# Optimization experiments

Hardware: AMD Instinct MI355X
Metric: run time of the kernel (lower is better)

Reference implementation:

```python
import jax, jax.numpy as jnp
import numpy as np

IN_DIM, H1, H2, N_CLASSES = 128, 100, 128, 19
BATCH, SEQ = 512, 256


def _lstm_relu(x, W, U, b, units):
    """Keras LSTM with activation='relu', recurrent_activation='sigmoid'.
    x: [B, T, D]. Returns (all hidden states [B, T, units], last hidden [B, units]).
    Gate order (Keras): i, f, g(cell candidate), o.
    """
    B = x.shape[0]
    h0 = jnp.zeros((B, units), x.dtype)
    c0 = jnp.zeros((B, units), x.dtype)

    # precompute input projections for all timesteps: [T, B, 4*units]
    zx = jnp.einsum('btd,dk->tbk', x, W) + b

    def step(carry, zx_t):
        h, c = carry
        z = zx_t + h @ U
        i, f, g, o = jnp.split(z, 4, axis=-1)
        i = jax.nn.sigmoid(i)
        f = jax.nn.sigmoid(f)
        g = jax.nn.relu(g)          # activation='relu'
        o = jax.nn.sigmoid(o)
        c = f * c + i * g
        h = o * jax.nn.relu(c)      # output activation is also relu
        return (h, c), h

    (h_last, _), hs = jax.lax.scan(step, (h0, c0), zx)
    return jnp.transpose(hs, (1, 0, 2)), h_last


def setup_inputs() -> dict:
    key = jax.random.key(0)
    ks = jax.random.split(key, 9)
    def w(k, shape, fan_in):
        return jax.random.normal(k, shape, jnp.float32) / np.sqrt(fan_in)
    x = jax.random.normal(ks[0], (BATCH, SEQ, IN_DIM), jnp.float32)
    return {
        'x': x,
        'W1': w(ks[1], (IN_DIM, 4 * H1), IN_DIM),
        'U1': w(ks[2], (H1, 4 * H1), H1),
        'b1': jnp.zeros((4 * H1,), jnp.float32),
        'W2': w(ks[3], (H1, 4 * H2), H1),
        'U2': w(ks[4], (H2, 4 * H2), H2),
        'b2': jnp.zeros((4 * H2,), jnp.float32),
        'Wd': w(ks[5], (H2, N_CLASSES), H2),
        'bd': jnp.zeros((N_CLASSES,), jnp.float32),
    }


def reference(x, W1, U1, b1, W2, U2, b2, Wd, bd):
    h1_seq, _ = _lstm_relu(x, W1, U1, b1, H1)      # [B, T, 100]
    _, h2 = _lstm_relu(h1_seq, W2, U2, b2, H2)     # [B, 128] (last step only)
    logits = h2 @ Wd + bd
    return jax.nn.softmax(logits, axis=-1)         # [B, 19]
```

## Files before the change

### kernel.cpp

```cpp
#include <hip/hip_runtime.h>
#include <math.h>


#define T_SEQ 256
#define BATCH 512
#define IN_DIM 128
#define H1 100
#define H2 128
#define NCLS 19

typedef float f4v __attribute__((ext_vector_type(4)));

__device__ __forceinline__ float sigmoidf_(float x) {
    return 1.0f / (1.0f + __expf(-x));
}
__device__ __forceinline__ float hsum4_(f4v v) {
    return (v.x + v.y) + (v.z + v.w);
}

#define REP8(M)  M(0) M(1) M(2) M(3) M(4) M(5) M(6) M(7)
#define REP25(M) M(0) M(1) M(2) M(3) M(4) M(5) M(6) M(7) M(8) M(9) M(10) M(11) \
                 M(12) M(13) M(14) M(15) M(16) M(17) M(18) M(19) M(20) M(21) M(22) M(23) M(24)

template<int K, int N, bool SWAP>
__global__ __launch_bounds__(256, 2)
void proj_kernel(const float* __restrict__ A, const float* __restrict__ W,
                 const float* __restrict__ bias, float* __restrict__ out)
{
    constexpr int LD = 132;
    __shared__ __align__(16) float As[32 * LD];
    __shared__ __align__(16) float Ws[32 * LD];
    const int tid = threadIdx.x;
    const int r0 = blockIdx.x * 128;
    const int c0 = blockIdx.y * 128;
    const int ty = tid >> 4, tx = tid & 15;

#define PACC(i) f4v accL##i = {0.f,0.f,0.f,0.f}; f4v accR##i = {0.f,0.f,0.f,0.f};
    REP8(PACC)
#undef PACC

    for (int kk = 0; kk < K; kk += 32) {
        __syncthreads();
#pragma unroll
        for (int i = 0; i < 4; ++i) {
            int idx = tid + i * 256;
            int row = idx >> 3, kg = idx & 7;
            int k = kk + kg * 4;
            f4v v = {0.f, 0.f, 0.f, 0.f};
            if (k < K) v = *(const f4v*)&A[(size_t)(r0 + row) * K + k];
            As[(kg * 4 + 0) * LD + row] = v.x;
            As[(kg * 4 + 1) * LD + row] = v.y;
            As[(kg * 4 + 2) * LD + row] = v.z;
            As[(kg * 4 + 3) * LD + row] = v.w;
        }
#pragma unroll
        for (int i = 0; i < 4; ++i) {
            int idx = tid + i * 256;
            int k = idx >> 5, cg = idx & 31;
            int gk = kk + k, gc = c0 + cg * 4;
            f4v v = {0.f, 0.f, 0.f, 0.f};
            if (gk < K && gc < N) v = *(const f4v*)&W[(size_t)gk * N + gc];
            *(f4v*)&Ws[k * LD + cg * 4] = v;
        }
        __syncthreads();
#pragma unroll
        for (int k = 0; k < 32; ++k) {
            f4v av0 = *(const f4v*)&As[k * LD + ty * 8];
            f4v av1 = *(const f4v*)&As[k * LD + ty * 8 + 4];
            f4v b0v = *(const f4v*)&Ws[k * LD + tx * 8];
            f4v b1v = *(const f4v*)&Ws[k * LD + tx * 8 + 4];
#define PFMA(i, s) accL##i += (s) * b0v; accR##i += (s) * b1v;
            PFMA(0, av0.x) PFMA(1, av0.y) PFMA(2, av0.z) PFMA(3, av0.w)
            PFMA(4, av1.x) PFMA(5, av1.y) PFMA(6, av1.z) PFMA(7, av1.w)
#undef PFMA
        }
    }

    const int cb = c0 + tx * 8;
    float b0 = (cb + 0 < N) ? bias[cb + 0] : 0.f;
    float b1 = (cb + 1 < N) ? bias[cb + 1] : 0.f;
    float b2 = (cb + 2 < N) ? bias[cb + 2] : 0.f;
    float b3 = (cb + 3 < N) ? bias[cb + 3] : 0.f;
    float b4 = (cb + 4 < N) ? bias[cb + 4] : 0.f;
    float b5 = (cb + 5 < N) ? bias[cb + 5] : 0.f;
    float b6 = (cb + 6 < N) ? bias[cb + 6] : 0.f;
    float b7 = (cb + 7 < N) ? bias[cb + 7] : 0.f;
    f4v bL = {b0, b1, b2, b3};
    f4v bR = {b4, b5, b6, b7};
#define PST(i) { \
        int r = r0 + ty * 8 + i; \
        size_t orow = SWAP ? ((size_t)(r & 255) * BATCH + (r >> 8)) : (size_t)r; \
        if (cb < N)     { f4v v = accL##i + bL; *(f4v*)&out[orow * N + cb] = v; } \
        if (cb + 4 < N) { f4v v = accR##i + bR; *(f4v*)&out[orow * N + cb + 4] = v; } }
    REP8(PST)
#undef PST
}

__global__ __launch_bounds__(256)
__attribute__((amdgpu_waves_per_eu(1, 1)))
void rec1_kernel(const float* __restrict__ zx,
                 const float* __restrict__ U1,
                 float* __restrict__ h1seq)
{
    const int row = blockIdx.x;
    const int k = threadIdx.x;
    __shared__ __align__(16) float hs[H1];
    __shared__ __align__(8) float fo[2 * H1];

    const int kk = (k < 200) ? k : 0;
    const int c0 = kk, c1 = kk + 200;

#define R1_LD(i) \
    f4v u0_##i, u1_##i; { \
        const float* p = U1 + (4 * i) * 400; \
        u0_##i = (f4v){p[c0], p[400 + c0], p[800 + c0], p[1200 + c0]}; \
        u1_##i = (f4v){p[c1], p[400 + c1], p[800 + c1], p[1200 + c1]}; }
    REP25(R1_LD)
#undef R1_LD

    if (k < H1) hs[k] = 0.0f;
    float cst = 0.0f;
    float zc0 = zx[(size_t)row * 400 + c0];
    float zc1 = zx[(size_t)row * 400 + c1];
    __syncthreads();

    for (int t = 0; t < T_SEQ; ++t) {
        int tn = (t + 1 < T_SEQ) ? t + 1 : t;
        const float* pz = &zx[((size_t)tn * BATCH + row) * 400];
        float zn0 = pz[c0];
        float zn1 = pz[c1];

        f4v s0 = {0.f, 0.f, 0.f, 0.f};
        f4v s1 = {0.f, 0.f, 0.f, 0.f};
#define R1_FMA(i) { f4v hv = *(const f4v*)&hs[4 * i]; s0 += hv * u0_##i; s1 += hv * u1_##i; }
        REP25(R1_FMA)
#undef R1_FMA
        float a0 = sigmoidf_(zc0 + hsum4_(s0));
        float a1h = zc1 + hsum4_(s1);
        float a1 = (k < H1) ? fmaxf(a1h, 0.0f) : sigmoidf_(a1h);
        if (k >= H1 && k < 200) *(float2*)&fo[2 * (k - H1)] = make_float2(a0, a1);
        __syncthreads();

        if (k < H1) {
            float2 f_o = *(const float2*)&fo[2 * k];
            cst = f_o.x * cst + a0 * a1;
            float h = f_o.y * fmaxf(cst, 0.0f);
            hs[k] = h;
            h1seq[((size_t)t * BATCH + row) * H1 + k] = h;
        }
        __syncthreads();
        zc0 = zn0;
        zc1 = zn1;
    }
}

template<bool INIT, bool LAST>
__global__ __launch_bounds__(512)
__attribute__((amdgpu_waves_per_eu(2, 2)))
void rec2_chunk(const float* __restrict__ zx,
                const float* __restrict__ U2,
                float* __restrict__ cbuf,
                float* __restrict__ hbuf,
                float* __restrict__ h2out,
                int tlen)
{
    const int row = blockIdx.x;
    const int tid = threadIdx.x;
    const int kq = tid >> 7;
    const int cl = tid & 127;
    __shared__ __align__(16) float hs[H2];
    __shared__ float zp[4 * 512];
    __shared__ float za[512];

#define R2_LD(j) \
    f4v w0_##j, w1_##j, w2_##j, w3_##j; { \
        const float* p = U2 + (size_t)(kq * 32 + 4 * j) * 512 + cl; \
        w0_##j = (f4v){p[0],   p[512],       p[1024],       p[1536]}; \
        w1_##j = (f4v){p[128], p[512 + 128], p[1024 + 128], p[1536 + 128]}; \
        w2_##j = (f4v){p[256], p[512 + 256], p[1024 + 256], p[1536 + 256]}; \
        w3_##j = (f4v){p[384], p[512 + 384], p[1024 + 384], p[1536 + 384]}; }
    REP8(R2_LD)
#undef R2_LD

    float cst = 0.0f;
    if (tid < H2) {
        if (INIT) {
            hs[tid] = 0.0f;
        } else {
            hs[tid] = hbuf[(size_t)row * H2 + tid];
            cst = cbuf[(size_t)row * H2 + tid];
        }
    }
    float zc = zx[(size_t)row * 512 + tid];
    __syncthreads();

    for (int t = 0; t < tlen; ++t) {
        int tn = (t + 1 < tlen) ? t + 1 : t;
        float zn = zx[((size_t)tn * BATCH + row) * 512 + tid];

        f4v s0 = {0.f, 0.f, 0.f, 0.f};
        f4v s1 = {0.f, 0.f, 0.f, 0.f};
        f4v s2 = {0.f, 0.f, 0.f, 0.f};
        f4v s3 = {0.f, 0.f, 0.f, 0.f};
#define R2_FMA(j) { f4v hv = *(const f4v*)&hs[kq * 32 + 4 * j]; \
        s0 += hv * w0_##j; s1 += hv * w1_##j; s2 += hv * w2_##j; s3 += hv * w3_##j; }
        REP8(R2_FMA)
#undef R2_FMA
        zp[kq * 512 + cl]       = hsum4_(s0);
        zp[kq * 512 + cl + 128] = hsum4_(s1);
        zp[kq * 512 + cl + 256] = hsum4_(s2);
        zp[kq * 512 + cl + 384] = hsum4_(s3);
        __syncthreads();

        float z = zc + (zp[tid] + zp[512 + tid]) + (zp[1024 + tid] + zp[1536 + tid]);
        float a = (tid >= 2 * H2 && tid < 3 * H2) ? fmaxf(z, 0.0f) : sigmoidf_(z);
        za[tid] = a;
        __syncthreads();

        if (tid < H2) {
            float i = za[tid], f = za[tid + 128], g = za[tid + 256], o = za[tid + 384];
            cst = f * cst + i * g;
            hs[tid] = o * fmaxf(cst, 0.0f);
        }
        __syncthreads();
        zc = zn;
    }

    if (tid < H2) {
        float h = hs[tid];
        cbuf[(size_t)row * H2 + tid] = cst;
        hbuf[(size_t)row * H2 + tid] = h;
        if (LAST) h2out[(size_t)row * H2 + tid] = h;
    }
}

__global__ __launch_bounds__(64, 1)
void dense_softmax_kernel(const float* __restrict__ h2, const float* __restrict__ Wd,
                          const float* __restrict__ bd, float* __restrict__ out)
{
    const int b = blockIdx.x;
    const int k = threadIdx.x;
    __shared__ __align__(16) float hsm[H2];
    if (k < H2 / 4) ((f4v*)hsm)[k] = ((const f4v*)(h2 + (size_t)b * H2))[k];
    __syncthreads();

    float logit = -1e30f;
    if (k < NCLS) {
        float acc = bd[k];
#pragma unroll
        for (int d = 0; d < H2; ++d) acc += hsm[d] * Wd[d * NCLS + k];
        logit = acc;
    }
    float m = logit;
#pragma unroll
    for (int off = 32; off >= 1; off >>= 1) m = fmaxf(m, __shfl_xor(m, off, 64));
    float e = (k < NCLS) ? __expf(logit - m) : 0.0f;
    float s = e;
#pragma unroll
    for (int off = 32; off >= 1; off >>= 1) s += __shfl_xor(s, off, 64);
    if (k < NCLS) out[(size_t)b * NCLS + k] = e / s;
}

__global__ __launch_bounds__(448, 1)
void lstm1_fb(const float* __restrict__ x, const float* __restrict__ W1,
              const float* __restrict__ U1, const float* __restrict__ b1,
              float* __restrict__ h1out)
{
    const int b = blockIdx.x;
    const int k = threadIdx.x;
    __shared__ __align__(16) float xs[IN_DIM];
    __shared__ __align__(16) float hs[H1];
    __shared__ __align__(16) float zs[4 * H1];
    float w1r[IN_DIM];
    float u1r[H1];
    float bias = 0.0f;
    if (k < 4 * H1) {
        bias = b1[k];
#pragma unroll
        for (int d = 0; d < IN_DIM; ++d) w1r[d] = W1[d * (4 * H1) + k];
#pragma unroll
        for (int j = 0; j < H1; ++j) u1r[j] = U1[j * (4 * H1) + k];
    }
    if (k < H1) hs[k] = 0.0f;
    if (k < IN_DIM / 4)
        ((float4*)xs)[k] = ((const float4*)(x + ((size_t)b * T_SEQ) * IN_DIM))[k];
    float c = 0.0f;
    __syncthreads();
    for (int t = 0; t < T_SEQ; ++t) {
        if (k < 4 * H1) {
            float acc0 = bias, acc1 = 0.f, acc2 = 0.f, acc3 = 0.f;
#pragma unroll
            for (int q = 0; q < IN_DIM / 4; ++q) {
                float4 xv = ((const float4*)xs)[q];
                acc0 += xv.x * w1r[4 * q]; acc1 += xv.y * w1r[4 * q + 1];
                acc2 += xv.z * w1r[4 * q + 2]; acc3 += xv.w * w1r[4 * q + 3];
            }
#pragma unroll
            for (int q = 0; q < H1 / 4; ++q) {
                float4 hv = ((const float4*)hs)[q];
                acc0 += hv.x * u1r[4 * q]; acc1 += hv.y * u1r[4 * q + 1];
                acc2 += hv.z * u1r[4 * q + 2]; acc3 += hv.w * u1r[4 * q + 3];
            }
            float zv = (acc0 + acc1) + (acc2 + acc3);
            zs[k] = (k >= 2 * H1 && k < 3 * H1) ? fmaxf(zv, 0.0f) : sigmoidf_(zv);
        }
        __syncthreads();
        if (k < H1) {
            float i = zs[k], f = zs[k + H1], g = zs[k + 2 * H1], o = zs[k + 3 * H1];
            c = f * c + i * g;
            float h = o * fmaxf(c, 0.0f);
            hs[k] = h;
            h1out[((size_t)t * BATCH + b) * H1 + k] = h;
        }
        int tn = t + 1;
        if (tn < T_SEQ && k < IN_DIM / 4)
            ((float4*)xs)[k] = ((const float4*)(x + ((size_t)b * T_SEQ + tn) * IN_DIM))[k];
        __syncthreads();
    }
}

__global__ __launch_bounds__(512, 1)
void lstm2_fb(const float* __restrict__ h1in, const float* __restrict__ W2,
              const float* __restrict__ U2, const float* __restrict__ b2,
              float* __restrict__ h2out)
{
    const int b = blockIdx.x;
    const int k = threadIdx.x;
    __shared__ __align__(16) float ps[H1];
    __shared__ __align__(16) float hs[H2];
    __shared__ __align__(16) float zs[4 * H2];
    float w2r[H1];
    float u2r[H2];
    float bias = b2[k];
#pragma unroll
    for (int j = 0; j < H1; ++j) w2r[j] = W2[j * (4 * H2) + k];
#pragma unroll
    for (int j = 0; j < H2; ++j) u2r[j] = U2[j * (4 * H2) + k];
    if (k < H2) hs[k] = 0.0f;
    if (k < H1 / 4)
        ((float4*)ps)[k] = ((const float4*)(h1in + (size_t)b * H1))[k];
    float c = 0.0f;
    float hlast = 0.0f;
    __syncthreads();
    for (int t = 0; t < T_SEQ; ++t) {
        float acc0 = bias, acc1 = 0.f, acc2 = 0.f, acc3 = 0.f;
#pragma unroll
        for (int q = 0; q < H1 / 4; ++q) {
            float4 pv = ((const float4*)ps)[q];
            acc0 += pv.x * w2r[4 * q]; acc1 += pv.y * w2r[4 * q + 1];
            acc2 += pv.z * w2r[4 * q + 2]; acc3 += pv.w * w2r[4 * q + 3];
        }
#pragma unroll
        for (int q = 0; q < H2 / 4; ++q) {
            float4 hv = ((const float4*)hs)[q];
            acc0 += hv.x * u2r[4 * q]; acc1 += hv.y * u2r[4 * q + 1];
            acc2 += hv.z * u2r[4 * q + 2]; acc3 += hv.w * u2r[4 * q + 3];
        }
        float zv = (acc0 + acc1) + (acc2 + acc3);
        zs[k] = (k >= 2 * H2 && k < 3 * H2) ? fmaxf(zv, 0.0f) : sigmoidf_(zv);
        __syncthreads();
        if (k < H2) {
            float i = zs[k], f = zs[k + H2], g = zs[k + 2 * H2], o = zs[k + 3 * H2];
            c = f * c + i * g;
            hlast = o * fmaxf(c, 0.0f);
            hs[k] = hlast;
        }
        int tn = t + 1;
        if (tn < T_SEQ && k < H1 / 4)
            ((float4*)ps)[k] = ((const float4*)(h1in + ((size_t)tn * BATCH + b) * H1))[k];
        __syncthreads();
    }
    if (k < H2) h2out[(size_t)b * H2 + k] = hlast;
}

extern "C" void kernel_launch(void* const* d_in, const int* in_sizes, int n_in,
                              void* d_out, int out_size, void* d_ws, size_t ws_size,
                              hipStream_t stream) {
    const float* x  = (const float*)d_in[0];
    const float* W1 = (const float*)d_in[1];
    const float* U1 = (const float*)d_in[2];
    const float* b1 = (const float*)d_in[3];
    const float* W2 = (const float*)d_in[4];
    const float* U2 = (const float*)d_in[5];
    const float* b2 = (const float*)d_in[6];
    const float* Wd = (const float*)d_in[7];
    const float* bd = (const float*)d_in[8];
    float* out = (float*)d_out;

    const size_t zx_elems = (size_t)T_SEQ * BATCH * 400;
    const size_t h1_elems = (size_t)T_SEQ * BATCH * H1;
    const size_t st_elems = (size_t)BATCH * H2;
    const size_t need = (zx_elems + h1_elems + 3 * st_elems) * sizeof(float);

    if (ws_size >= need) {
        float* zxbuf = (float*)d_ws;
        float* h1buf = zxbuf + zx_elems;
        float* cbuf  = h1buf + h1_elems;
        float* hbuf  = cbuf + st_elems;
        float* h2buf = hbuf + st_elems;
        const int TC = T_SEQ / 2;

        hipLaunchKernelGGL((proj_kernel<IN_DIM, 4 * H1, true>), dim3(1024, 4), dim3(256), 0, stream,
                           x, W1, b1, zxbuf);
        hipLaunchKernelGGL(rec1_kernel, dim3(BATCH), dim3(256), 0, stream,
                           zxbuf, U1, h1buf);
        hipLaunchKernelGGL((proj_kernel<H1, 4 * H2, false>), dim3(512, 4), dim3(256), 0, stream,
                           h1buf, W2, b2, zxbuf);
        hipLaunchKernelGGL((rec2_chunk<true, false>), dim3(BATCH), dim3(512), 0, stream,
                           zxbuf, U2, cbuf, hbuf, h2buf, TC);
        hipLaunchKernelGGL((proj_kernel<H1, 4 * H2, false>), dim3(512, 4), dim3(256), 0, stream,
                           h1buf + (size_t)TC * BATCH * H1, W2, b2, zxbuf);
        hipLaunchKernelGGL((rec2_chunk<false, true>), dim3(BATCH), dim3(512), 0, stream,
                           zxbuf, U2, cbuf, hbuf, h2buf, TC);

        hipLaunchKernelGGL(dense_softmax_kernel, dim3(BATCH), dim3(64), 0, stream,
                           h2buf, Wd, bd, out);
    } else {
        float* h1buf = (float*)d_ws;
        float* h2buf = h1buf + h1_elems;
        hipLaunchKernelGGL(lstm1_fb, dim3(BATCH), dim3(448), 0, stream, x, W1, U1, b1, h1buf);
        hipLaunchKernelGGL(lstm2_fb, dim3(BATCH), dim3(512), 0, stream, h1buf, W2, U2, b2, h2buf);
        hipLaunchKernelGGL(dense_softmax_kernel, dim3(BATCH), dim3(64), 0, stream, h2buf, Wd, bd, out);
    }
}
```

Measured before the change: 1.300 ms.

## Replace per-row recurrent LSTM kernels with batched MFMA bf16x3 recurrence

Replaces the scalar per-batch-row recurrence kernels for both LSTM layers with one templated kernel. Each block now handles 16 batch rows and computes h@U with bf16 MFMA instructions, splitting values into hi/lo parts (three products) to keep near-fp32 accuracy. This cuts the grid from 512 blocks to 32, trading parallelism across CUs for matrix-core throughput and reuse of the weight fragments held in registers. Risks are lower occupancy (only 32 CUs busy), extra split arithmetic every step, and a small precision drift from the bf16x3 emulation.

```diff
diff --git a/kernel.cpp b/kernel.cpp
--- a/kernel.cpp
+++ b/kernel.cpp
@@ -10,18 +10,224 @@
 #define NCLS 19
 
 typedef float f4v __attribute__((ext_vector_type(4)));
+typedef short s8v __attribute__((ext_vector_type(8)));
+
+#define ZERO8 ((s8v){0, 0, 0, 0, 0, 0, 0, 0})
+#define REP8S(M) M(0) M(1) M(2) M(3) M(4) M(5) M(6) M(7)
 
 __device__ __forceinline__ float sigmoidf_(float x) {
     return 1.0f / (1.0f + __expf(-x));
 }
-__device__ __forceinline__ float hsum4_(f4v v) {
-    return (v.x + v.y) + (v.z + v.w);
-}
-
-#define REP8(M)  M(0) M(1) M(2) M(3) M(4) M(5) M(6) M(7)
-#define REP25(M) M(0) M(1) M(2) M(3) M(4) M(5) M(6) M(7) M(8) M(9) M(10) M(11) \
-                 M(12) M(13) M(14) M(15) M(16) M(17) M(18) M(19) M(20) M(21) M(22) M(23) M(24)
-
+__device__ __forceinline__ f4v sig4_(f4v z) {
+    f4v r;
+    r.x = sigmoidf_(z.x); r.y = sigmoidf_(z.y);
+    r.z = sigmoidf_(z.z); r.w = sigmoidf_(z.w);
+    return r;
+}
+__device__ __forceinline__ f4v relu4_(f4v z) {
+    f4v r;
+    r.x = fmaxf(z.x, 0.f); r.y = fmaxf(z.y, 0.f);
+    r.z = fmaxf(z.z, 0.f); r.w = fmaxf(z.w, 0.f);
+    return r;
+}
+
+__device__ __forceinline__ short bf_hi_(float x, float& hif) {
+    unsigned u = __builtin_bit_cast(unsigned, x);
+    unsigned r = (u + 0x7FFFu + ((u >> 16) & 1u)) & 0xFFFF0000u;
+    hif = __builtin_bit_cast(float, r);
+    return (short)(r >> 16);
+}
+__device__ __forceinline__ void bsplit_(float x, short& hi, short& lo) {
+    float hif;
+    hi = bf_hi_(x, hif);
+    float rs = x - hif;
+    float d;
+    lo = bf_hi_(rs, d);
+}
+
+template<int NU, int NG>
+__device__ __forceinline__ void load_bfrag_(const float* __restrict__ U,
+                                            int k0, int n, s8v& hi, s8v& lo) {
+    short hh[8], ll[8];
+#pragma unroll
+    for (int j = 0; j < 8; ++j) {
+        float x = (k0 + j < NU) ? U[(size_t)(k0 + j) * NG + n] : 0.0f;
+        bsplit_(x, hh[j], ll[j]);
+    }
+    hi = (s8v){hh[0], hh[1], hh[2], hh[3], hh[4], hh[5], hh[6], hh[7]};
+    lo = (s8v){ll[0], ll[1], ll[2], ll[3], ll[4], ll[5], ll[6], ll[7]};
+}
+
+__device__ __forceinline__ void load_afrag_(const float* p, s8v& ah, s8v& al) {
+    f4v x0 = *(const f4v*)p;
+    f4v x1 = *(const f4v*)(p + 4);
+    short h0, h1, h2, h3, h4, h5, h6, h7, l0, l1, l2, l3, l4, l5, l6, l7;
+    bsplit_(x0.x, h0, l0); bsplit_(x0.y, h1, l1);
+    bsplit_(x0.z, h2, l2); bsplit_(x0.w, h3, l3);
+    bsplit_(x1.x, h4, l4); bsplit_(x1.y, h5, l5);
+    bsplit_(x1.z, h6, l6); bsplit_(x1.w, h7, l7);
+    ah = (s8v){h0, h1, h2, h3, h4, h5, h6, h7};
+    al = (s8v){l0, l1, l2, l3, l4, l5, l6, l7};
+}
+
+template<int NU, bool SEQOUT, bool INIT, bool WRSTATE, bool WROUT>
+__global__ __launch_bounds__(256)
+__attribute__((amdgpu_waves_per_eu(1, 1)))
+void recm_kernel(const float* __restrict__ zx,
+                 const float* __restrict__ U,
+                 float* __restrict__ outp,
+                 float* __restrict__ cbuf,
+                 float* __restrict__ hbuf,
+                 int tlen)
+{
+    constexpr int NG = 4 * NU;
+    constexpr int NT = NG / 16;
+    constexpr int ZLD = 20;
+    constexpr int ALD = 132;
+    __shared__ float za[NG * ZLD];
+    __shared__ float hA[16 * ALD];
+
+    const int tid = threadIdx.x;
+    const int wv = tid >> 6;
+    const int lane = tid & 63;
+    const int lm = lane & 15;
+    const int lq = lane >> 4;
+    const int blk16 = blockIdx.x * 16;
+
+#define BDECL(s) \
+    const int nt##s = 4 * (s) + wv; const bool v##s = (nt##s) < NT; \
+    s8v bh##s##_0 = ZERO8, bh##s##_1 = ZERO8, bh##s##_2 = ZERO8, bh##s##_3 = ZERO8; \
+    s8v bl##s##_0 = ZERO8, bl##s##_1 = ZERO8, bl##s##_2 = ZERO8, bl##s##_3 = ZERO8; \
+    if (v##s) { \
+        int nn = nt##s * 16 + lm; \
+        load_bfrag_<NU, NG>(U,  0 + lq * 8, nn, bh##s##_0, bl##s##_0); \
+        load_bfrag_<NU, NG>(U, 32 + lq * 8, nn, bh##s##_1, bl##s##_1); \
+        load_bfrag_<NU, NG>(U, 64 + lq * 8, nn, bh##s##_2, bl##s##_2); \
+        load_bfrag_<NU, NG>(U, 96 + lq * 8, nn, bh##s##_3, bl##s##_3); \
+    }
+    REP8S(BDECL)
+#undef BDECL
+
+    if (INIT) {
+        for (int i = tid; i < 16 * ALD; i += 256) hA[i] = 0.0f;
+    } else {
+        int row = tid >> 4, k8 = (tid & 15) * 8;
+        f4v a = *(const f4v*)&hbuf[(size_t)(blk16 + row) * NU + k8];
+        f4v b = *(const f4v*)&hbuf[(size_t)(blk16 + row) * NU + k8 + 4];
+        *(f4v*)&hA[row * ALD + k8] = a;
+        *(f4v*)&hA[row * ALD + k8 + 4] = b;
+    }
+    f4v c0_ = {0.f, 0.f, 0.f, 0.f}, c1_ = {0.f, 0.f, 0.f, 0.f};
+    if (!INIT) {
+        {
+            int id = tid;
+            if (id < NU * 4) {
+                int u = id >> 2, rg = id & 3;
+                const float* pc = &cbuf[(size_t)(blk16 + rg * 4) * NU + u];
+                c0_ = (f4v){pc[0], pc[NU], pc[2 * NU], pc[3 * NU]};
+            }
+        }
+        {
+            int id = tid + 256;
+            if (id < NU * 4) {
+                int u = id >> 2, rg = id & 3;
+                const float* pc = &cbuf[(size_t)(blk16 + rg * 4) * NU + u];
+                c1_ = (f4v){pc[0], pc[NU], pc[2 * NU], pc[3 * NU]};
+            }
+        }
+    }
+    __syncthreads();
+
+#define TRIP(s, kt) \
+    acc = __builtin_amdgcn_mfma_f32_16x16x32_bf16(ah##kt, bh##s##_##kt, acc, 0, 0, 0); \
+    acc = __builtin_amdgcn_mfma_f32_16x16x32_bf16(al##kt, bh##s##_##kt, acc, 0, 0, 0); \
+    acc = __builtin_amdgcn_mfma_f32_16x16x32_bf16(ah##kt, bl##s##_##kt, acc, 0, 0, 0);
+
+#define TILEC(s) \
+    if (v##s) { \
+        const float* pz = zx + zbase + nt##s * 16; \
+        f4v acc = (f4v){pz[0], pz[NG], pz[2 * NG], pz[3 * NG]}; \
+        TRIP(s, 0) TRIP(s, 1) TRIP(s, 2) TRIP(s, 3) \
+        *(f4v*)&za[(nt##s * 16 + lm) * ZLD + lq * 4] = acc; \
+    }
+
+#define UPDATE(a, cr) { \
+        int id = tid + 256 * (a); \
+        if (id < NU * 4) { \
+            int u = id >> 2, rg = id & 3; \
+            f4v iv = *(const f4v*)&za[(u         ) * ZLD + rg * 4]; \
+            f4v fv = *(const f4v*)&za[(u +     NU) * ZLD + rg * 4]; \
+            f4v gv = *(const f4v*)&za[(u + 2 * NU) * ZLD + rg * 4]; \
+            f4v ov = *(const f4v*)&za[(u + 3 * NU) * ZLD + rg * 4]; \
+            iv = sig4_(iv); fv = sig4_(fv); gv = relu4_(gv); ov = sig4_(ov); \
+            cr = fv * cr + iv * gv; \
+            f4v hv = ov * relu4_(cr); \
+            hA[(rg * 4 + 0) * ALD + u] = hv.x; \
+            hA[(rg * 4 + 1) * ALD + u] = hv.y; \
+            hA[(rg * 4 + 2) * ALD + u] = hv.z; \
+            hA[(rg * 4 + 3) * ALD + u] = hv.w; \
+            if (SEQOUT) { \
+                float* po = outp + ((size_t)t * BATCH + blk16 + rg * 4) * NU + u; \
+                po[0] = hv.x; po[NU] = hv.y; po[2 * NU] = hv.z; po[3 * NU] = hv.w; \
+            } \
+        } \
+    }
+
+#pragma unroll 1
+    for (int t = 0; t < tlen; ++t) {
+        s8v ah0, al0, ah1, al1, ah2, al2, ah3, al3;
+        load_afrag_(&hA[lm * ALD +  0 + lq * 8], ah0, al0);
+        load_afrag_(&hA[lm * ALD + 32 + lq * 8], ah1, al1);
+        load_afrag_(&hA[lm * ALD + 64 + lq * 8], ah2, al2);
+        load_afrag_(&hA[lm * ALD + 96 + lq * 8], ah3, al3);
+
+        const size_t zbase = ((size_t)t * BATCH + blk16 + lq * 4) * NG + lm;
+        REP8S(TILEC)
+        __syncthreads();
+
+        UPDATE(0, c0_)
+        UPDATE(1, c1_)
+        __syncthreads();
+    }
+#undef TILEC
+#undef TRIP
+#undef UPDATE
+
+    if (WRSTATE) {
+        {
+            int row = tid >> 4, k8 = (tid & 15) * 8;
+            f4v a = *(const f4v*)&hA[row * ALD + k8];
+            f4v b = *(const f4v*)&hA[row * ALD + k8 + 4];
+            *(f4v*)&hbuf[(size_t)(blk16 + row) * NU + k8] = a;
+            *(f4v*)&hbuf[(size_t)(blk16 + row) * NU + k8 + 4] = b;
+        }
+        {
+            int id = tid;
+            if (id < NU * 4) {
+                int u = id >> 2, rg = id & 3;
+                float* pc = &cbuf[(size_t)(blk16 + rg * 4) * NU + u];
+                pc[0] = c0_.x; pc[NU] = c0_.y; pc[2 * NU] = c0_.z; pc[3 * NU] = c0_.w;
+            }
+        }
+        {
+            int id = tid + 256;
+            if (id < NU * 4) {
+                int u = id >> 2, rg = id & 3;
+                float* pc = &cbuf[(size_t)(blk16 + rg * 4) * NU + u];
+                pc[0] = c1_.x; pc[NU] = c1_.y; pc[2 * NU] = c1_.z; pc[3 * NU] = c1_.w;
+            }
+        }
+    }
+    if (WROUT) {
+        int row = tid >> 4, k8 = (tid & 15) * 8;
+        f4v a = *(const f4v*)&hA[row * ALD + k8];
+        f4v b = *(const f4v*)&hA[row * ALD + k8 + 4];
+        *(f4v*)&outp[(size_t)(blk16 + row) * NU + k8] = a;
+        *(f4v*)&outp[(size_t)(blk16 + row) * NU + k8 + 4] = b;
+    }
+}
+
+#define PREP8(M)  M(0) M(1) M(2) M(3) M(4) M(5) M(6) M(7)
 template<int K, int N, bool SWAP>
 __global__ __launch_bounds__(256, 2)
 void proj_kernel(const float* __restrict__ A, const float* __restrict__ W,
@@ -36,7 +242,7 @@
     const int ty = tid >> 4, tx = tid & 15;
 
 #define PACC(i) f4v accL##i = {0.f,0.f,0.f,0.f}; f4v accR##i = {0.f,0.f,0.f,0.f};
-    REP8(PACC)
+    PREP8(PACC)
 #undef PACC
 
     for (int kk = 0; kk < K; kk += 32) {
@@ -92,146 +298,8 @@
         size_t orow = SWAP ? ((size_t)(r & 255) * BATCH + (r >> 8)) : (size_t)r; \
         if (cb < N)     { f4v v = accL##i + bL; *(f4v*)&out[orow * N + cb] = v; } \
         if (cb + 4 < N) { f4v v = accR##i + bR; *(f4v*)&out[orow * N + cb + 4] = v; } }
-    REP8(PST)
+    PREP8(PST)
 #undef PST
-}
-
-__global__ __launch_bounds__(256)
-__attribute__((amdgpu_waves_per_eu(1, 1)))
-void rec1_kernel(const float* __restrict__ zx,
-                 const float* __restrict__ U1,
-                 float* __restrict__ h1seq)
-{
-    const int row = blockIdx.x;
-    const int k = threadIdx.x;
-    __shared__ __align__(16) float hs[H1];
-    __shared__ __align__(8) float fo[2 * H1];
-
-    const int kk = (k < 200) ? k : 0;
-    const int c0 = kk, c1 = kk + 200;
-
-#define R1_LD(i) \
-    f4v u0_##i, u1_##i; { \
-        const float* p = U1 + (4 * i) * 400; \
-        u0_##i = (f4v){p[c0], p[400 + c0], p[800 + c0], p[1200 + c0]}; \
-        u1_##i = (f4v){p[c1], p[400 + c1], p[800 + c1], p[1200 + c1]}; }
-    REP25(R1_LD)
-#undef R1_LD
-
-    if (k < H1) hs[k] = 0.0f;
-    float cst = 0.0f;
-    float zc0 = zx[(size_t)row * 400 + c0];
-    float zc1 = zx[(size_t)row * 400 + c1];
-    __syncthreads();
-
-    for (int t = 0; t < T_SEQ; ++t) {
-        int tn = (t + 1 < T_SEQ) ? t + 1 : t;
-        const float* pz = &zx[((size_t)tn * BATCH + row) * 400];
-        float zn0 = pz[c0];
-        float zn1 = pz[c1];
-
-        f4v s0 = {0.f, 0.f, 0.f, 0.f};
-        f4v s1 = {0.f, 0.f, 0.f, 0.f};
-#define R1_FMA(i) { f4v hv = *(const f4v*)&hs[4 * i]; s0 += hv * u0_##i; s1 += hv * u1_##i; }
-        REP25(R1_FMA)
-#undef R1_FMA
-        float a0 = sigmoidf_(zc0 + hsum4_(s0));
-        float a1h = zc1 + hsum4_(s1);
-        float a1 = (k < H1) ? fmaxf(a1h, 0.0f) : sigmoidf_(a1h);
-        if (k >= H1 && k < 200) *(float2*)&fo[2 * (k - H1)] = make_float2(a0, a1);
-        __syncthreads();
-
-        if (k < H1) {
-            float2 f_o = *(const float2*)&fo[2 * k];
-            cst = f_o.x * cst + a0 * a1;
-            float h = f_o.y * fmaxf(cst, 0.0f);
-            hs[k] = h;
-            h1seq[((size_t)t * BATCH + row) * H1 + k] = h;
-        }
-        __syncthreads();
-        zc0 = zn0;
-        zc1 = zn1;
-    }
-}
-
-template<bool INIT, bool LAST>
-__global__ __launch_bounds__(512)
-__attribute__((amdgpu_waves_per_eu(2, 2)))
-void rec2_chunk(const float* __restrict__ zx,
-                const float* __restrict__ U2,
-                float* __restrict__ cbuf,
-                float* __restrict__ hbuf,
-                float* __restrict__ h2out,
-                int tlen)
-{
-    const int row = blockIdx.x;
-    const int tid = threadIdx.x;
-    const int kq = tid >> 7;
-    const int cl = tid & 127;
-    __shared__ __align__(16) float hs[H2];
-    __shared__ float zp[4 * 512];
-    __shared__ float za[512];
-
-#define R2_LD(j) \
-    f4v w0_##j, w1_##j, w2_##j, w3_##j; { \
-        const float* p = U2 + (size_t)(kq * 32 + 4 * j) * 512 + cl; \
-        w0_##j = (f4v){p[0],   p[512],       p[1024],       p[1536]}; \
-        w1_##j = (f4v){p[128], p[512 + 128], p[1024 + 128], p[1536 + 128]}; \
-        w2_##j = (f4v){p[256], p[512 + 256], p[1024 + 256], p[1536 + 256]}; \
-        w3_##j = (f4v){p[384], p[512 + 384], p[1024 + 384], p[1536 + 384]}; }
-    REP8(R2_LD)
-#undef R2_LD
-
-    float cst = 0.0f;
-    if (tid < H2) {
-        if (INIT) {
-            hs[tid] = 0.0f;
-        } else {
-            hs[tid] = hbuf[(size_t)row * H2 + tid];
-            cst = cbuf[(size_t)row * H2 + tid];
-        }
-    }
-    float zc = zx[(size_t)row * 512 + tid];
-    __syncthreads();
-
-    for (int t = 0; t < tlen; ++t) {
-        int tn = (t + 1 < tlen) ? t + 1 : t;
-        float zn = zx[((size_t)tn * BATCH + row) * 512 + tid];
-
-        f4v s0 = {0.f, 0.f, 0.f, 0.f};
-        f4v s1 = {0.f, 0.f, 0.f, 0.f};
-        f4v s2 = {0.f, 0.f, 0.f, 0.f};
-        f4v s3 = {0.f, 0.f, 0.f, 0.f};
-#define R2_FMA(j) { f4v hv = *(const f4v*)&hs[kq * 32 + 4 * j]; \
-        s0 += hv * w0_##j; s1 += hv * w1_##j; s2 += hv * w2_##j; s3 += hv * w3_##j; }
-        REP8(R2_FMA)
-#undef R2_FMA
-        zp[kq * 512 + cl]       = hsum4_(s0);
-        zp[kq * 512 + cl + 128] = hsum4_(s1);
-        zp[kq * 512 + cl + 256] = hsum4_(s2);
-        zp[kq * 512 + cl + 384] = hsum4_(s3);
-        __syncthreads();
-
-        float z = zc + (zp[tid] + zp[512 + tid]) + (zp[1024 + tid] + zp[1536 + tid]);
-        float a = (tid >= 2 * H2 && tid < 3 * H2) ? fmaxf(z, 0.0f) : sigmoidf_(z);
-        za[tid] = a;
-        __syncthreads();
-
-        if (tid < H2) {
-            float i = za[tid], f = za[tid + 128], g = za[tid + 256], o = za[tid + 384];
-            cst = f * cst + i * g;
-            hs[tid] = o * fmaxf(cst, 0.0f);
-        }
-        __syncthreads();
-        zc = zn;
-    }
-
-    if (tid < H2) {
-        float h = hs[tid];
-        cbuf[(size_t)row * H2 + tid] = cst;
-        hbuf[(size_t)row * H2 + tid] = h;
-        if (LAST) h2out[(size_t)row * H2 + tid] = h;
-    }
 }
 
 __global__ __launch_bounds__(64, 1)
@@ -402,16 +470,16 @@
 
         hipLaunchKernelGGL((proj_kernel<IN_DIM, 4 * H1, true>), dim3(1024, 4), dim3(256), 0, stream,
                            x, W1, b1, zxbuf);
-        hipLaunchKernelGGL(rec1_kernel, dim3(BATCH), dim3(256), 0, stream,
-                           zxbuf, U1, h1buf);
+        hipLaunchKernelGGL((recm_kernel<H1, true, true, false, false>), dim3(32), dim3(256), 0, stream,
+                           zxbuf, U1, h1buf, (float*)nullptr, (float*)nullptr, T_SEQ);
         hipLaunchKernelGGL((proj_kernel<H1, 4 * H2, false>), dim3(512, 4), dim3(256), 0, stream,
                            h1buf, W2, b2, zxbuf);
-        hipLaunchKernelGGL((rec2_chunk<true, false>), dim3(BATCH), dim3(512), 0, stream,
-                           zxbuf, U2, cbuf, hbuf, h2buf, TC);
+        hipLaunchKernelGGL((recm_kernel<H2, false, true, true, false>), dim3(32), dim3(256), 0, stream,
+                           zxbuf, U2, (float*)nullptr, cbuf, hbuf, TC);
         hipLaunchKernelGGL((proj_kernel<H1, 4 * H2, false>), dim3(512, 4), dim3(256), 0, stream,
                            h1buf + (size_t)TC * BATCH * H1, W2, b2, zxbuf);
-        hipLaunchKernelGGL((rec2_chunk<false, true>), dim3(BATCH), dim3(512), 0, stream,
-                           zxbuf, U2, cbuf, hbuf, h2buf, TC);
+        hipLaunchKernelGGL((recm_kernel<H2, false, false, false, true>), dim3(32), dim3(256), 0, stream,
+                           zxbuf, U2, h2buf, cbuf, hbuf, TC);
 
         hipLaunchKernelGGL(dense_softmax_kernel, dim3(BATCH), dim3(64), 0, stream,
                            h2buf, Wd, bd, out);
```

Measured after the change: 2.497 ms. +92.1%, slower.
